# Kernel tuning notes

Measured on AMD Instinct MI355X. Metric: run time of the kernel, lower is better.

## Reference

```python
import jax, jax.numpy as jnp
import numpy as np

N = 100000
E = 1600000
IN_F, HID, OUT_F = 256, 128, 64


def setup_inputs() -> dict:
    key = jax.random.key(0)
    k_x, k_e, k_w1, k_w2, k_b1, k_b2 = jax.random.split(key, 6)
    x = jax.random.normal(k_x, (N, IN_F), dtype=jnp.float32)
    edge_index = jax.random.randint(k_e, (2, E), 0, N, dtype=jnp.int32)
    # GCNConv params: lin has no bias in PyG; separate additive bias per layer.
    W1 = jax.random.normal(k_w1, (IN_F, HID), dtype=jnp.float32) / np.sqrt(IN_F)
    b1 = jax.random.normal(k_b1, (HID,), dtype=jnp.float32) * 0.01
    W2 = jax.random.normal(k_w2, (HID, OUT_F), dtype=jnp.float32) / np.sqrt(HID)
    b2 = jax.random.normal(k_b2, (OUT_F,), dtype=jnp.float32) * 0.01
    return {"x": x, "edge_index": edge_index, "W1": W1, "b1": b1, "W2": W2, "b2": b2}


def _gcn_norm(edge_index, num_nodes):
    # add self loops (improved=False -> weight 1.0), symmetric normalization
    loop = jnp.arange(num_nodes, dtype=edge_index.dtype)
    src = jnp.concatenate([edge_index[0], loop])
    dst = jnp.concatenate([edge_index[1], loop])
    w = jnp.ones(src.shape[0], dtype=jnp.float32)
    deg = jax.ops.segment_sum(w, dst, num_segments=num_nodes)
    dinv = jnp.where(deg > 0, jax.lax.rsqrt(deg), 0.0)
    norm = dinv[src] * w * dinv[dst]
    return src, dst, norm


def _gcn_layer(h, W, b, src, dst, norm, num_nodes):
    h = h @ W                               # [N, out]
    msg = h[src] * norm[:, None]            # [E+N, out] gather + scale
    out = jax.ops.segment_sum(msg, dst, num_segments=num_nodes)  # scatter-add
    return out + b


def reference(x, edge_index, W1, b1, W2, b2):
    # dropout is identity in eval mode
    src, dst, norm = _gcn_norm(edge_index, N)
    h = _gcn_layer(x, W1, b1, src, dst, norm, N)
    h = jax.nn.relu(h)
    out = _gcn_layer(h, W2, b2, src, dst, norm, N)
    return out
```

## Files before the change

### kernel.cpp

```cpp
#include <hip/hip_runtime.h>
#include <hip/hip_bf16.h>

#define N_NODES 100000
#define N_EDGES 1600000
#define IN_FEAT 256
#define HID_F   128
#define OUT_FT  64

#define NBUK   128
#define NPB    782
#define BUKCAP 16384
#define EPB    8192
#define G_BIN  ((N_EDGES + EPB - 1) / EPB)
#define G_GEMM ((N_NODES + 127) / 128)
#define G_CAST ((IN_FEAT * HID_F + HID_F * OUT_FT + 255) / 256)

typedef unsigned short u16;
typedef __attribute__((ext_vector_type(8))) unsigned short u16x8;
typedef __attribute__((ext_vector_type(8))) short short8;
typedef __attribute__((ext_vector_type(4))) float f32x4;

static __device__ inline u16 f2bf(float f) {
    __hip_bfloat16 h = __float2bfloat16(f);
    return *reinterpret_cast<u16*>(&h);
}


__global__ __launch_bounds__(256) void k_bin(const int* __restrict__ srcA,
                                             const int* __restrict__ dstA,
                                             int* __restrict__ gcur, int2* __restrict__ pairs,
                                             const float* __restrict__ W1,
                                             const float* __restrict__ W2,
                                             u16* __restrict__ W1t, u16* __restrict__ W2t) {
    if (blockIdx.x >= G_BIN) {
        int idx = (blockIdx.x - G_BIN) * 256 + threadIdx.x;
        if (idx < IN_FEAT * HID_F) {
            int k = idx / HID_F, n = idx % HID_F;
            W1t[n * IN_FEAT + k] = f2bf(W1[idx]);
        } else {
            int e2 = idx - IN_FEAT * HID_F;
            if (e2 < HID_F * OUT_FT) {
                int k = e2 / OUT_FT, n = e2 % OUT_FT;
                W2t[n * HID_F + k] = f2bf(W2[e2]);
            }
        }
        return;
    }
    __shared__ int lh[NBUK];
    int t = threadIdx.x;
    int e0 = blockIdx.x * EPB;
    if (t < NBUK) lh[t] = 0;
    __syncthreads();
#pragma unroll
    for (int i = 0; i < EPB / 256; i++) {
        int e = e0 + i * 256 + t;
        if (e < N_EDGES) atomicAdd(&lh[dstA[e] / NPB], 1);
    }
    __syncthreads();
    if (t < NBUK) {
        int c = lh[t];
        lh[t] = atomicAdd(&gcur[t], c);
    }
    __syncthreads();
#pragma unroll
    for (int i = 0; i < EPB / 256; i++) {
        int e = e0 + i * 256 + t;
        if (e < N_EDGES) {
            int d = dstA[e];
            int b = d / NPB;
            int p = atomicAdd(&lh[b], 1);
            if (p < BUKCAP) pairs[(size_t)b * BUKCAP + p] = make_int2(srcA[e], d);
        }
    }
}


__global__ __launch_bounds__(256) void k_bukscan(const int* __restrict__ gcur,
                                                 int* __restrict__ bbase) {
    __shared__ int sm[256];
    int t = threadIdx.x;
    int v = (t < NBUK) ? gcur[t] : 0;
    sm[t] = v;
    __syncthreads();
    for (int o = 1; o < 256; o <<= 1) {
        int u = (t >= o) ? sm[t - o] : 0;
        __syncthreads();
        sm[t] += u;
        __syncthreads();
    }
    if (t < NBUK) bbase[t] = sm[t] - v;
    if (t == NBUK - 1) bbase[NBUK] = sm[t];
}


__global__ __launch_bounds__(256) void k_fillB(const int2* __restrict__ pairs,
                                               const int* __restrict__ gcnt,
                                               const int* __restrict__ bbase,
                                               int* __restrict__ offsets,
                                               float* __restrict__ dinv,
                                               int* __restrict__ csr) {
    __shared__ int hist[NPB];
    __shared__ int sm[256];
    int b = blockIdx.x, t = threadIdx.x;
    int nbase = b * NPB;
    int nn = min(NPB, N_NODES - nbase);
    int cnt = gcnt[b];
    int ebase = bbase[b];
    const int2* pb = pairs + (size_t)b * BUKCAP;

    for (int i = t; i < NPB; i += 256) hist[i] = 0;
    __syncthreads();
    for (int i = t; i < cnt; i += 256) atomicAdd(&hist[pb[i].y - nbase], 1);
    __syncthreads();

    int base4 = t * 4;
    int c0 = 0, c1 = 0, c2 = 0, c3 = 0;
    if (base4 < NPB) {
        c0 = hist[base4];
        c1 = (base4 + 1 < NPB) ? hist[base4 + 1] : 0;
        c2 = (base4 + 2 < NPB) ? hist[base4 + 2] : 0;
        c3 = (base4 + 3 < NPB) ? hist[base4 + 3] : 0;
    }
    int s = c0 + c1 + c2 + c3;
    sm[t] = s;
    __syncthreads();
    for (int o = 1; o < 256; o <<= 1) {
        int u = (t >= o) ? sm[t - o] : 0;
        __syncthreads();
        sm[t] += u;
        __syncthreads();
    }
    int run = ebase + sm[t] - s;
    __syncthreads();
    int cc[4] = {c0, c1, c2, c3};
#pragma unroll
    for (int q = 0; q < 4; q++) {
        int n = base4 + q;
        if (n < nn) {
            int g = nbase + n;
            offsets[g] = run;
            dinv[g] = rsqrtf((float)(cc[q] + 1));
            hist[n] = run;
            run += cc[q];
        }
    }
    __syncthreads();
    for (int i = t; i < cnt; i += 256) {
        int2 e = pb[i];
        int p = atomicAdd(&hist[e.y - nbase], 1);
        csr[p] = e.x;
    }
    if (b == NBUK - 1 && t == 0) offsets[N_NODES] = N_EDGES;
}


__global__ __launch_bounds__(256) void k_gemm1(const float* __restrict__ A,
                                               const u16* __restrict__ Bt,
                                               const float* __restrict__ dinv,
                                               u16* __restrict__ C) {
    __shared__ u16 As[128][40];
    __shared__ u16 Bs[128][40];
    int tid = threadIdx.x;
    int wv = tid >> 6, lane = tid & 63;
    int m16 = lane & 15, quad = lane >> 4;
    int row0 = blockIdx.x * 128;
    int r = tid >> 1, h = tid & 1;
    int grow_s = row0 + r;
    bool rok = grow_s < N_NODES;

    f32x4 acc[2][8];
#pragma unroll
    for (int i = 0; i < 2; i++)
#pragma unroll
        for (int j = 0; j < 8; j++) acc[i][j] = (f32x4)(0.f);

    for (int k0 = 0; k0 < IN_FEAT; k0 += 32) {
        f32x4 v0 = (f32x4)(0.f), v1 = v0, v2 = v0, v3 = v0;
        if (rok) {
            const f32x4* src = (const f32x4*)&A[(size_t)grow_s * IN_FEAT + k0 + h * 16];
            v0 = src[0]; v1 = src[1]; v2 = src[2]; v3 = src[3];
        }
        u16x8 p0, p1;
#pragma unroll
        for (int j = 0; j < 4; j++) {
            p0[j] = f2bf(v0[j]); p0[4 + j] = f2bf(v1[j]);
            p1[j] = f2bf(v2[j]); p1[4 + j] = f2bf(v3[j]);
        }
        *(u16x8*)&As[r][h * 16] = p0;
        *(u16x8*)&As[r][h * 16 + 8] = p1;
        const u16x8* bsrc = (const u16x8*)&Bt[(size_t)r * IN_FEAT + k0 + h * 16];
        *(u16x8*)&Bs[r][h * 16] = bsrc[0];
        *(u16x8*)&Bs[r][h * 16 + 8] = bsrc[1];
        __syncthreads();

        short8 af0 = *(const short8*)&As[32 * wv + m16][quad * 8];
        short8 af1 = *(const short8*)&As[32 * wv + 16 + m16][quad * 8];
#pragma unroll
        for (int ct = 0; ct < 8; ct++) {
            short8 bf = *(const short8*)&Bs[16 * ct + m16][quad * 8];
            acc[0][ct] = __builtin_amdgcn_mfma_f32_16x16x32_bf16(af0, bf, acc[0][ct], 0, 0, 0);
            acc[1][ct] = __builtin_amdgcn_mfma_f32_16x16x32_bf16(af1, bf, acc[1][ct], 0, 0, 0);
        }
        __syncthreads();
    }
#pragma unroll
    for (int rt = 0; rt < 2; rt++)
#pragma unroll
        for (int r4 = 0; r4 < 4; r4++) {
            int grow = row0 + 32 * wv + 16 * rt + quad * 4 + r4;
            if (grow < N_NODES) {
                float dv = dinv[grow];
#pragma unroll
                for (int ct = 0; ct < 8; ct++)
                    C[(size_t)grow * HID_F + 16 * ct + m16] = f2bf(acc[rt][ct][r4] * dv);
            }
        }
}


__global__ __launch_bounds__(256) void k_gemm2(const u16* __restrict__ A,
                                               const u16* __restrict__ Bt,
                                               const float* __restrict__ dinv,
                                               u16* __restrict__ C) {
    __shared__ u16 As[128][40];
    __shared__ u16 Bs[64][40];
    int tid = threadIdx.x;
    int wv = tid >> 6, lane = tid & 63;
    int m16 = lane & 15, quad = lane >> 4;
    int row0 = blockIdx.x * 128;
    int r = tid >> 1, h = tid & 1;
    int grow_s = row0 + r;
    bool rok = grow_s < N_NODES;
    int nb = tid >> 2, q = tid & 3;

    f32x4 acc[2][4];
#pragma unroll
    for (int i = 0; i < 2; i++)
#pragma unroll
        for (int j = 0; j < 4; j++) acc[i][j] = (f32x4)(0.f);

    for (int k0 = 0; k0 < HID_F; k0 += 32) {
        u16x8 a0 = (u16x8)(0), a1v = (u16x8)(0);
        if (rok) {
            const u16x8* src = (const u16x8*)&A[(size_t)grow_s * HID_F + k0 + h * 16];
            a0 = src[0]; a1v = src[1];
        }
        *(u16x8*)&As[r][h * 16] = a0;
        *(u16x8*)&As[r][h * 16 + 8] = a1v;
        *(u16x8*)&Bs[nb][q * 8] = *(const u16x8*)&Bt[(size_t)nb * HID_F + k0 + q * 8];
        __syncthreads();

        short8 af0 = *(const short8*)&As[32 * wv + m16][quad * 8];
        short8 af1 = *(const short8*)&As[32 * wv + 16 + m16][quad * 8];
#pragma unroll
        for (int ct = 0; ct < 4; ct++) {
            short8 bf = *(const short8*)&Bs[16 * ct + m16][quad * 8];
            acc[0][ct] = __builtin_amdgcn_mfma_f32_16x16x32_bf16(af0, bf, acc[0][ct], 0, 0, 0);
            acc[1][ct] = __builtin_amdgcn_mfma_f32_16x16x32_bf16(af1, bf, acc[1][ct], 0, 0, 0);
        }
        __syncthreads();
    }
#pragma unroll
    for (int rt = 0; rt < 2; rt++)
#pragma unroll
        for (int r4 = 0; r4 < 4; r4++) {
            int grow = row0 + 32 * wv + 16 * rt + quad * 4 + r4;
            if (grow < N_NODES) {
                float dv = dinv[grow];
#pragma unroll
                for (int ct = 0; ct < 4; ct++)
                    C[(size_t)grow * OUT_FT + 16 * ct + m16] = f2bf(acc[rt][ct][r4] * dv);
            }
        }
}


__global__ __launch_bounds__(256) void k_agg1(const u16* __restrict__ hs,
                                              const int* __restrict__ offsets,
                                              const int* __restrict__ csr,
                                              const float* __restrict__ dinv,
                                              const float* __restrict__ b,
                                              u16* __restrict__ out) {
    int wave = threadIdx.x >> 6;
    int lane = threadIdx.x & 63;
    int node = blockIdx.x * 4 + wave;
    if (node >= N_NODES) return;
    int beg = offsets[node], end = offsets[node + 1];
    float2 acc = __bfloat1622float2(*(const __hip_bfloat162*)&hs[(size_t)node * HID_F + lane * 2]);
    int j = beg;
    for (; j + 8 <= end; j += 8) {
        int s0 = csr[j], s1 = csr[j + 1], s2 = csr[j + 2], s3 = csr[j + 3];
        int s4 = csr[j + 4], s5 = csr[j + 5], s6 = csr[j + 6], s7 = csr[j + 7];
        float2 v0 = __bfloat1622float2(*(const __hip_bfloat162*)&hs[(size_t)s0 * HID_F + lane * 2]);
        float2 v1 = __bfloat1622float2(*(const __hip_bfloat162*)&hs[(size_t)s1 * HID_F + lane * 2]);
        float2 v2 = __bfloat1622float2(*(const __hip_bfloat162*)&hs[(size_t)s2 * HID_F + lane * 2]);
        float2 v3 = __bfloat1622float2(*(const __hip_bfloat162*)&hs[(size_t)s3 * HID_F + lane * 2]);
        float2 v4 = __bfloat1622float2(*(const __hip_bfloat162*)&hs[(size_t)s4 * HID_F + lane * 2]);
        float2 v5 = __bfloat1622float2(*(const __hip_bfloat162*)&hs[(size_t)s5 * HID_F + lane * 2]);
        float2 v6 = __bfloat1622float2(*(const __hip_bfloat162*)&hs[(size_t)s6 * HID_F + lane * 2]);
        float2 v7 = __bfloat1622float2(*(const __hip_bfloat162*)&hs[(size_t)s7 * HID_F + lane * 2]);
        acc.x += ((v0.x + v1.x) + (v2.x + v3.x)) + ((v4.x + v5.x) + (v6.x + v7.x));
        acc.y += ((v0.y + v1.y) + (v2.y + v3.y)) + ((v4.y + v5.y) + (v6.y + v7.y));
    }
    for (; j < end; j++) {
        float2 v = __bfloat1622float2(*(const __hip_bfloat162*)&hs[(size_t)csr[j] * HID_F + lane * 2]);
        acc.x += v.x;
        acc.y += v.y;
    }
    float dv = dinv[node];
    float2 bb = *(const float2*)&b[lane * 2];
    float ox = fmaxf(dv * acc.x + bb.x, 0.f);
    float oy = fmaxf(dv * acc.y + bb.y, 0.f);
    __hip_bfloat162 ob = __float22bfloat162_rn(make_float2(ox, oy));
    *(__hip_bfloat162*)&out[(size_t)node * HID_F + lane * 2] = ob;
}

__global__ __launch_bounds__(256) void k_agg2(const u16* __restrict__ hs,
                                              const int* __restrict__ offsets,
                                              const int* __restrict__ csr,
                                              const float* __restrict__ dinv,
                                              const float* __restrict__ b,
                                              float* __restrict__ out) {
    int wave = threadIdx.x >> 6;
    int lane = threadIdx.x & 63;
    int node = blockIdx.x * 4 + wave;
    if (node >= N_NODES) return;
    int beg = offsets[node], end = offsets[node + 1];
    float acc = __bfloat162float(*(const __hip_bfloat16*)&hs[(size_t)node * OUT_FT + lane]);
    int j = beg;
    for (; j + 8 <= end; j += 8) {
        int s0 = csr[j], s1 = csr[j + 1], s2 = csr[j + 2], s3 = csr[j + 3];
        int s4 = csr[j + 4], s5 = csr[j + 5], s6 = csr[j + 6], s7 = csr[j + 7];
        float v0 = __bfloat162float(*(const __hip_bfloat16*)&hs[(size_t)s0 * OUT_FT + lane]);
        float v1 = __bfloat162float(*(const __hip_bfloat16*)&hs[(size_t)s1 * OUT_FT + lane]);
        float v2 = __bfloat162float(*(const __hip_bfloat16*)&hs[(size_t)s2 * OUT_FT + lane]);
        float v3 = __bfloat162float(*(const __hip_bfloat16*)&hs[(size_t)s3 * OUT_FT + lane]);
        float v4 = __bfloat162float(*(const __hip_bfloat16*)&hs[(size_t)s4 * OUT_FT + lane]);
        float v5 = __bfloat162float(*(const __hip_bfloat16*)&hs[(size_t)s5 * OUT_FT + lane]);
        float v6 = __bfloat162float(*(const __hip_bfloat16*)&hs[(size_t)s6 * OUT_FT + lane]);
        float v7 = __bfloat162float(*(const __hip_bfloat16*)&hs[(size_t)s7 * OUT_FT + lane]);
        acc += ((v0 + v1) + (v2 + v3)) + ((v4 + v5) + (v6 + v7));
    }
    for (; j < end; j++)
        acc += __bfloat162float(*(const __hip_bfloat16*)&hs[(size_t)csr[j] * OUT_FT + lane]);
    out[(size_t)node * OUT_FT + lane] = dinv[node] * acc + b[lane];
}


extern "C" void kernel_launch(void* const* d_in, const int* in_sizes, int n_in,
                              void* d_out, int out_size, void* d_ws, size_t ws_size,
                              hipStream_t stream) {
    const float* x  = (const float*)d_in[0];
    const int*   ei = (const int*)d_in[1];
    const float* W1 = (const float*)d_in[2];
    const float* b1 = (const float*)d_in[3];
    const float* W2 = (const float*)d_in[4];
    const float* b2 = (const float*)d_in[5];
    float* out = (float*)d_out;

    char* ws = (char*)d_ws;
    int*   offsets = (int*)(ws + 0);
    float* dinv    = (float*)(ws + 400512);
    int*   csr     = (int*)(ws + 800512);
    u16*   W1t     = (u16*)(ws + 7200512);
    u16*   W2t     = (u16*)(ws + 7266048);
    int*   gcur    = (int*)(ws + 7282432);
    int*   bbase   = (int*)(ws + 7282944);
    u16*   hs1     = (u16*)(ws + 7283968);
    u16*   a1      = (u16*)(ws + 32883968);
    int2*  pairs   = (int2*)(ws + 32883968);
    u16*   hs2     = hs1;

    const int* srcA = ei;
    const int* dstA = ei + N_EDGES;

    hipMemsetAsync(gcur, 0, NBUK * sizeof(int), stream);

    k_bin<<<G_BIN + G_CAST, 256, 0, stream>>>(srcA, dstA, gcur, pairs, W1, W2, W1t, W2t);
    k_bukscan<<<1, 256, 0, stream>>>(gcur, bbase);
    k_fillB<<<NBUK, 256, 0, stream>>>(pairs, gcur, bbase, offsets, dinv, csr);

    k_gemm1<<<G_GEMM, 256, 0, stream>>>(x, W1t, dinv, hs1);
    k_agg1<<<(N_NODES + 3) / 4, 256, 0, stream>>>(hs1, offsets, csr, dinv, b1, a1);
    k_gemm2<<<G_GEMM, 256, 0, stream>>>(a1, W2t, dinv, hs2);
    k_agg2<<<(N_NODES + 3) / 4, 256, 0, stream>>>(hs2, offsets, csr, dinv, b2, out);
}
```

Before: 405.9 us.

## Vectorize neighbor gathers with 16-byte row loads and split edges across lane groups

After: 356.4 us. -12.2%, faster.

```diff
diff --git a/kernel.cpp b/kernel.cpp
--- a/kernel.cpp
+++ b/kernel.cpp
@@ -7,10 +7,10 @@
 #define HID_F   128
 #define OUT_FT  64
 
-#define NBUK   128
-#define NPB    782
-#define BUKCAP 16384
-#define EPB    8192
+#define NBUK   256
+#define NPB    391
+#define BUKCAP 8192
+#define EPB    4096
 #define G_BIN  ((N_EDGES + EPB - 1) / EPB)
 #define G_GEMM ((N_NODES + 127) / 128)
 #define G_CAST ((IN_FEAT * HID_F + HID_F * OUT_FT + 255) / 256)
@@ -23,6 +23,11 @@
 static __device__ inline u16 f2bf(float f) {
     __hip_bfloat16 h = __float2bfloat16(f);
     return *reinterpret_cast<u16*>(&h);
+}
+static __device__ inline float bf2f(u16 u) {
+    union { unsigned u; float f; } c;
+    c.u = ((unsigned)u) << 16;
+    return c.f;
 }
 
 
@@ -79,7 +84,7 @@
                                                  int* __restrict__ bbase) {
     __shared__ int sm[256];
     int t = threadIdx.x;
-    int v = (t < NBUK) ? gcur[t] : 0;
+    int v = gcur[t];
     sm[t] = v;
     __syncthreads();
     for (int o = 1; o < 256; o <<= 1) {
@@ -88,7 +93,7 @@
         sm[t] += u;
         __syncthreads();
     }
-    if (t < NBUK) bbase[t] = sm[t] - v;
+    bbase[t] = sm[t] - v;
     if (t == NBUK - 1) bbase[NBUK] = sm[t];
 }
 
@@ -113,15 +118,10 @@
     for (int i = t; i < cnt; i += 256) atomicAdd(&hist[pb[i].y - nbase], 1);
     __syncthreads();
 
-    int base4 = t * 4;
-    int c0 = 0, c1 = 0, c2 = 0, c3 = 0;
-    if (base4 < NPB) {
-        c0 = hist[base4];
-        c1 = (base4 + 1 < NPB) ? hist[base4 + 1] : 0;
-        c2 = (base4 + 2 < NPB) ? hist[base4 + 2] : 0;
-        c3 = (base4 + 3 < NPB) ? hist[base4 + 3] : 0;
-    }
-    int s = c0 + c1 + c2 + c3;
+    int base2 = t * 2;
+    int c0 = (base2 < NPB) ? hist[base2] : 0;
+    int c1 = (base2 + 1 < NPB) ? hist[base2 + 1] : 0;
+    int s = c0 + c1;
     sm[t] = s;
     __syncthreads();
     for (int o = 1; o < 256; o <<= 1) {
@@ -132,10 +132,10 @@
     }
     int run = ebase + sm[t] - s;
     __syncthreads();
-    int cc[4] = {c0, c1, c2, c3};
-#pragma unroll
-    for (int q = 0; q < 4; q++) {
-        int n = base4 + q;
+    int cc[2] = {c0, c1};
+#pragma unroll
+    for (int q = 0; q < 2; q++) {
+        int n = base2 + q;
         if (n < nn) {
             int g = nbase + n;
             offsets[g] = run;
@@ -285,35 +285,56 @@
     int lane = threadIdx.x & 63;
     int node = blockIdx.x * 4 + wave;
     if (node >= N_NODES) return;
+    int g = lane >> 4;
+    int fl = lane & 15;
+    const int fo = fl * 8;
     int beg = offsets[node], end = offsets[node + 1];
-    float2 acc = __bfloat1622float2(*(const __hip_bfloat162*)&hs[(size_t)node * HID_F + lane * 2]);
+
+    float acc[8];
+#pragma unroll
+    for (int i = 0; i < 8; i++) acc[i] = 0.f;
+
     int j = beg;
     for (; j + 8 <= end; j += 8) {
-        int s0 = csr[j], s1 = csr[j + 1], s2 = csr[j + 2], s3 = csr[j + 3];
-        int s4 = csr[j + 4], s5 = csr[j + 5], s6 = csr[j + 6], s7 = csr[j + 7];
-        float2 v0 = __bfloat1622float2(*(const __hip_bfloat162*)&hs[(size_t)s0 * HID_F + lane * 2]);
-        float2 v1 = __bfloat1622float2(*(const __hip_bfloat162*)&hs[(size_t)s1 * HID_F + lane * 2]);
-        float2 v2 = __bfloat1622float2(*(const __hip_bfloat162*)&hs[(size_t)s2 * HID_F + lane * 2]);
-        float2 v3 = __bfloat1622float2(*(const __hip_bfloat162*)&hs[(size_t)s3 * HID_F + lane * 2]);
-        float2 v4 = __bfloat1622float2(*(const __hip_bfloat162*)&hs[(size_t)s4 * HID_F + lane * 2]);
-        float2 v5 = __bfloat1622float2(*(const __hip_bfloat162*)&hs[(size_t)s5 * HID_F + lane * 2]);
-        float2 v6 = __bfloat1622float2(*(const __hip_bfloat162*)&hs[(size_t)s6 * HID_F + lane * 2]);
-        float2 v7 = __bfloat1622float2(*(const __hip_bfloat162*)&hs[(size_t)s7 * HID_F + lane * 2]);
-        acc.x += ((v0.x + v1.x) + (v2.x + v3.x)) + ((v4.x + v5.x) + (v6.x + v7.x));
-        acc.y += ((v0.y + v1.y) + (v2.y + v3.y)) + ((v4.y + v5.y) + (v6.y + v7.y));
-    }
-    for (; j < end; j++) {
-        float2 v = __bfloat1622float2(*(const __hip_bfloat162*)&hs[(size_t)csr[j] * HID_F + lane * 2]);
-        acc.x += v.x;
-        acc.y += v.y;
-    }
-    float dv = dinv[node];
-    float2 bb = *(const float2*)&b[lane * 2];
-    float ox = fmaxf(dv * acc.x + bb.x, 0.f);
-    float oy = fmaxf(dv * acc.y + bb.y, 0.f);
-    __hip_bfloat162 ob = __float22bfloat162_rn(make_float2(ox, oy));
-    *(__hip_bfloat162*)&out[(size_t)node * HID_F + lane * 2] = ob;
-}
+        int s0 = csr[j + g];
+        int s1 = csr[j + 4 + g];
+        u16x8 r0 = *(const u16x8*)&hs[(size_t)s0 * HID_F + fo];
+        u16x8 r1 = *(const u16x8*)&hs[(size_t)s1 * HID_F + fo];
+#pragma unroll
+        for (int i = 0; i < 8; i++) acc[i] += bf2f(r0[i]) + bf2f(r1[i]);
+    }
+    for (; j < end; j += 4) {
+        int idx = j + g;
+        if (idx < end) {
+            int s = csr[idx];
+            u16x8 r0 = *(const u16x8*)&hs[(size_t)s * HID_F + fo];
+#pragma unroll
+            for (int i = 0; i < 8; i++) acc[i] += bf2f(r0[i]);
+        }
+    }
+#pragma unroll
+    for (int i = 0; i < 8; i++) {
+        acc[i] += __shfl_xor(acc[i], 16, 64);
+        acc[i] += __shfl_xor(acc[i], 32, 64);
+    }
+    u16x8 sr = *(const u16x8*)&hs[(size_t)node * HID_F + fo];
+#pragma unroll
+    for (int i = 0; i < 8; i++) acc[i] += bf2f(sr[i]);
+
+    if (g == 0) {
+        float dv = dinv[node];
+        f32x4 b0 = *(const f32x4*)&b[fo];
+        f32x4 b1 = *(const f32x4*)&b[fo + 4];
+        u16x8 o;
+#pragma unroll
+        for (int i = 0; i < 4; i++) {
+            o[i] = f2bf(fmaxf(dv * acc[i] + b0[i], 0.f));
+            o[4 + i] = f2bf(fmaxf(dv * acc[4 + i] + b1[i], 0.f));
+        }
+        *(u16x8*)&out[(size_t)node * HID_F + fo] = o;
+    }
+}
+
 
 __global__ __launch_bounds__(256) void k_agg2(const u16* __restrict__ hs,
                                               const int* __restrict__ offsets,
@@ -325,25 +346,56 @@
     int lane = threadIdx.x & 63;
     int node = blockIdx.x * 4 + wave;
     if (node >= N_NODES) return;
+    int g = lane >> 3;
+    int fl = lane & 7;
+    const int fo = fl * 8;
     int beg = offsets[node], end = offsets[node + 1];
-    float acc = __bfloat162float(*(const __hip_bfloat16*)&hs[(size_t)node * OUT_FT + lane]);
+
+    float acc[8];
+#pragma unroll
+    for (int i = 0; i < 8; i++) acc[i] = 0.f;
+
     int j = beg;
-    for (; j + 8 <= end; j += 8) {
-        int s0 = csr[j], s1 = csr[j + 1], s2 = csr[j + 2], s3 = csr[j + 3];
-        int s4 = csr[j + 4], s5 = csr[j + 5], s6 = csr[j + 6], s7 = csr[j + 7];
-        float v0 = __bfloat162float(*(const __hip_bfloat16*)&hs[(size_t)s0 * OUT_FT + lane]);
-        float v1 = __bfloat162float(*(const __hip_bfloat16*)&hs[(size_t)s1 * OUT_FT + lane]);
-        float v2 = __bfloat162float(*(const __hip_bfloat16*)&hs[(size_t)s2 * OUT_FT + lane]);
-        float v3 = __bfloat162float(*(const __hip_bfloat16*)&hs[(size_t)s3 * OUT_FT + lane]);
-        float v4 = __bfloat162float(*(const __hip_bfloat16*)&hs[(size_t)s4 * OUT_FT + lane]);
-        float v5 = __bfloat162float(*(const __hip_bfloat16*)&hs[(size_t)s5 * OUT_FT + lane]);
-        float v6 = __bfloat162float(*(const __hip_bfloat16*)&hs[(size_t)s6 * OUT_FT + lane]);
-        float v7 = __bfloat162float(*(const __hip_bfloat16*)&hs[(size_t)s7 * OUT_FT + lane]);
-        acc += ((v0 + v1) + (v2 + v3)) + ((v4 + v5) + (v6 + v7));
-    }
-    for (; j < end; j++)
-        acc += __bfloat162float(*(const __hip_bfloat16*)&hs[(size_t)csr[j] * OUT_FT + lane]);
-    out[(size_t)node * OUT_FT + lane] = dinv[node] * acc + b[lane];
+    for (; j + 16 <= end; j += 16) {
+        int s0 = csr[j + g];
+        int s1 = csr[j + 8 + g];
+        u16x8 r0 = *(const u16x8*)&hs[(size_t)s0 * OUT_FT + fo];
+        u16x8 r1 = *(const u16x8*)&hs[(size_t)s1 * OUT_FT + fo];
+#pragma unroll
+        for (int i = 0; i < 8; i++) acc[i] += bf2f(r0[i]) + bf2f(r1[i]);
+    }
+    for (; j < end; j += 8) {
+        int idx = j + g;
+        if (idx < end) {
+            int s = csr[idx];
+            u16x8 r0 = *(const u16x8*)&hs[(size_t)s * OUT_FT + fo];
+#pragma unroll
+            for (int i = 0; i < 8; i++) acc[i] += bf2f(r0[i]);
+        }
+    }
+#pragma unroll
+    for (int i = 0; i < 8; i++) {
+        acc[i] += __shfl_xor(acc[i], 8, 64);
+        acc[i] += __shfl_xor(acc[i], 16, 64);
+        acc[i] += __shfl_xor(acc[i], 32, 64);
+    }
+    u16x8 sr = *(const u16x8*)&hs[(size_t)node * OUT_FT + fo];
+#pragma unroll
+    for (int i = 0; i < 8; i++) acc[i] += bf2f(sr[i]);
+
+    if (g == 0) {
+        float dv = dinv[node];
+        f32x4 b0 = *(const f32x4*)&b[fo];
+        f32x4 b1 = *(const f32x4*)&b[fo + 4];
+        f32x4 o0, o1;
+#pragma unroll
+        for (int i = 0; i < 4; i++) {
+            o0[i] = dv * acc[i] + b0[i];
+            o1[i] = dv * acc[4 + i] + b1[i];
+        }
+        *(f32x4*)&out[(size_t)node * OUT_FT + fo] = o0;
+        *(f32x4*)&out[(size_t)node * OUT_FT + fo + 4] = o1;
+    }
 }
 
 
@@ -365,10 +417,10 @@
     u16*   W1t     = (u16*)(ws + 7200512);
     u16*   W2t     = (u16*)(ws + 7266048);
     int*   gcur    = (int*)(ws + 7282432);
-    int*   bbase   = (int*)(ws + 7282944);
-    u16*   hs1     = (u16*)(ws + 7283968);
-    u16*   a1      = (u16*)(ws + 32883968);
-    int2*  pairs   = (int2*)(ws + 32883968);
+    int*   bbase   = (int*)(ws + 7283456);
+    u16*   hs1     = (u16*)(ws + 7284608);
+    u16*   a1      = (u16*)(ws + 32884608);
+    int2*  pairs   = (int2*)(ws + 32884608);
     u16*   hs2     = hs1;
 
     const int* srcA = ei;
```
